# Kernel tuning notes

Hardware: AMD Instinct MI355X
Metric: run time of the kernel (lower is better)

The kernel has to match this reference:

```python
import jax, jax.numpy as jnp
import numpy as np

B, C, T, S, E = 8, 1024, 2048, 2048, 1024
SCALE = 0.7071067811865476  # sqrt(0.5), as in ConvS2S


def setup_inputs() -> dict:
    key = jax.random.key(0)
    ks = jax.random.split(key, 8)
    return {
        "conved": jax.random.normal(ks[0], (B, C, T), jnp.float32),
        "encoder_conved": jax.random.normal(ks[1], (B, S, E), jnp.float32),
        "encoder_combined": jax.random.normal(ks[2], (B, S, E), jnp.float32),
        "x": jax.random.normal(ks[3], (B, T, E), jnp.float32),
        "scale": jnp.float32(SCALE),
        # attn_hid2emb: Linear(out_channels -> emb_dim); torch weight is [out, in]
        "W_h2e": jax.random.normal(ks[4], (E, C), jnp.float32) * 0.02,
        "b_h2e": jnp.zeros((E,), jnp.float32),
        # attn_emb2hid: Linear(emb_dim -> out_channels)
        "W_e2h": jax.random.normal(ks[5], (C, E), jnp.float32) * 0.02,
        "b_e2h": jnp.zeros((C,), jnp.float32),
    }


def reference(conved, encoder_conved, encoder_combined, x, scale,
              W_h2e, b_h2e, W_e2h, b_e2h):
    # conved: [B, C, T] -> project to embedding space: [B, T, E]
    conved_emb = jnp.einsum('bct,ec->bte', conved, W_h2e) + b_h2e
    conved_combined = (conved_emb + x) * scale            # [B, T, E]
    # energy = Q @ K^T : [B, T, S]
    energy = jnp.einsum('bte,bse->bts', conved_combined, encoder_conved)
    attention = jax.nn.softmax(energy, axis=-1)           # [B, T, S]
    # attended encoding = A @ V : [B, T, E]
    attended = jnp.einsum('bts,bse->bte', attention, encoder_combined)
    # project back to hidden: [B, T, C]
    attended = jnp.einsum('bte,ce->btc', attended, W_e2h) + b_e2h
    # residual in channels-first layout: [B, C, T]
    attended_combined = conved + attended.transpose(0, 2, 1)
    return attention, attended_combined
```

## Files before the change

### kernel.cpp

```cpp
#include <hip/hip_runtime.h>
#include <hip/hip_bf16.h>

typedef unsigned short u16;
typedef __attribute__((ext_vector_type(8))) short bf16x8;
typedef __attribute__((ext_vector_type(4))) float f32x4;

#define B_ 8
#define C_ 1024
#define T_ 2048
#define S_ 2048
#define E_ 1024

__device__ __forceinline__ u16 f2bf(float v) {
    __hip_bfloat16 h = __float2bfloat16(v);
    return *reinterpret_cast<u16*>(&h);
}
__device__ __forceinline__ float bf2f(u16 u) {
    __hip_bfloat16 h = *reinterpret_cast<__hip_bfloat16*>(&u);
    return __bfloat162float(h);
}
__device__ __forceinline__ void split2(float v, u16& h, u16& l) {
    h = f2bf(v);
    l = f2bf(v - bf2f(h));
}

__device__ __forceinline__ void async16(const u16* g, u16* l) {
    __builtin_amdgcn_global_load_lds((const __attribute__((address_space(1))) void*)g,
                                     (__attribute__((address_space(3))) void*)l, 16, 0, 0);
}

template<int EPI, bool SPLIT3>
__global__ __launch_bounds__(256, 4) void gemm_bt(
    const u16* __restrict__ Ahi, const u16* __restrict__ Alo,
    const u16* __restrict__ Bhi, const u16* __restrict__ Blo,
    int Kdim, long sA, long sB, int N,
    float* __restrict__ outF, long sOutF,
    u16* __restrict__ outB, u16* __restrict__ outB2, long sOutB,
    const float* __restrict__ bias,
    const float* __restrict__ add, long sAdd,
    const float* __restrict__ scale_ptr)
{
    __shared__ u16 smem[(SPLIT3 ? 4 : 2) * 4096];
    u16* As_hi = smem;
    u16* Bs_hi = smem + 4096;
    u16* As_lo = SPLIT3 ? (smem + 8192)  : smem;
    u16* Bs_lo = SPLIT3 ? (smem + 12288) : smem;

    const int gx = gridDim.x;
    const int nwg = gx * gridDim.y;
    int f = blockIdx.y * gx + blockIdx.x;
    {
        const int q = nwg >> 3, r = nwg & 7;
        const int xcd = f & 7, idx = f >> 3;
        f = (xcd < r ? xcd * (q + 1) : r * (q + 1) + (xcd - r) * q) + idx;
    }
    const int b  = blockIdx.z;
    const int bm = (f / gx) * 128;
    const int bn = (f % gx) * 128;

    const u16* Ah = Ahi + (size_t)b * sA;
    const u16* Bh = Bhi + (size_t)b * sB;
    const u16* Al = SPLIT3 ? (Alo + (size_t)b * sA) : nullptr;
    const u16* Bl = SPLIT3 ? (Blo + (size_t)b * sB) : nullptr;

    const int tid  = threadIdx.x;
    const int w    = tid >> 6, lane = tid & 63;
    const int wr   = w >> 1,   wc   = w & 1;
    const int lr   = lane & 15, ls  = lane >> 4;

    const int srow  = lane >> 2;
    const int sslot = lane & 3;
    const int kk    = ((sslot ^ ((srow >> 1) & 3)) << 3);
    const size_t gA0 = (size_t)(bm + w * 16 + srow) * Kdim + kk;
    const size_t gA1 = (size_t)(bm + (w + 4) * 16 + srow) * Kdim + kk;
    const size_t gB0 = (size_t)(bn + w * 16 + srow) * Kdim + kk;
    const size_t gB1 = (size_t)(bn + (w + 4) * 16 + srow) * Kdim + kk;
    const int l0 = w * 512, l1 = (w + 4) * 512;

    f32x4 acc[4][4];
    #pragma unroll
    for (int m = 0; m < 4; m++) {
        #pragma unroll
        for (int n = 0; n < 4; n++) {
            f32x4 z = {0.f, 0.f, 0.f, 0.f};
            acc[m][n] = z;
        }
    }

    const int foff = ((ls ^ ((lr >> 1) & 3)) << 3);

    for (int k0 = 0; k0 < Kdim; k0 += 32) {
        async16(Ah + gA0 + k0, As_hi + l0);
        async16(Ah + gA1 + k0, As_hi + l1);
        async16(Bh + gB0 + k0, Bs_hi + l0);
        async16(Bh + gB1 + k0, Bs_hi + l1);
        if constexpr (SPLIT3) {
            async16(Al + gA0 + k0, As_lo + l0);
            async16(Al + gA1 + k0, As_lo + l1);
            async16(Bl + gB0 + k0, Bs_lo + l0);
            async16(Bl + gB1 + k0, Bs_lo + l1);
        }
        asm volatile("s_waitcnt vmcnt(0)" ::: "memory");
        __syncthreads();

        bf16x8 ah[4], al[4];
        #pragma unroll
        for (int m = 0; m < 4; m++) {
            int off = (wr * 64 + m * 16 + lr) * 32 + foff;
            ah[m] = *(const bf16x8*)(As_hi + off);
            if constexpr (SPLIT3) al[m] = *(const bf16x8*)(As_lo + off);
        }
        #pragma unroll
        for (int n = 0; n < 4; n++) {
            int off = (wc * 64 + n * 16 + lr) * 32 + foff;
            bf16x8 bh = *(const bf16x8*)(Bs_hi + off);
            if constexpr (SPLIT3) {
                bf16x8 bl = *(const bf16x8*)(Bs_lo + off);
                #pragma unroll
                for (int m = 0; m < 4; m++)
                    acc[m][n] = __builtin_amdgcn_mfma_f32_16x16x32_bf16(ah[m], bh, acc[m][n], 0, 0, 0);
                #pragma unroll
                for (int m = 0; m < 4; m++)
                    acc[m][n] = __builtin_amdgcn_mfma_f32_16x16x32_bf16(ah[m], bl, acc[m][n], 0, 0, 0);
                #pragma unroll
                for (int m = 0; m < 4; m++)
                    acc[m][n] = __builtin_amdgcn_mfma_f32_16x16x32_bf16(al[m], bh, acc[m][n], 0, 0, 0);
            } else {
                #pragma unroll
                for (int m = 0; m < 4; m++)
                    acc[m][n] = __builtin_amdgcn_mfma_f32_16x16x32_bf16(ah[m], bh, acc[m][n], 0, 0, 0);
            }
        }
        __syncthreads();
    }

    float scl = 1.0f;
    if constexpr (EPI == 0) scl = *scale_ptr;

    #pragma unroll
    for (int m = 0; m < 4; m++) {
        #pragma unroll
        for (int n = 0; n < 4; n++) {
            const int Rb = bm + wr * 64 + m * 16 + ls * 4;
            const int Cc = bn + wc * 64 + n * 16 + lr;
            f32x4 v = acc[m][n];
            #pragma unroll
            for (int j = 0; j < 4; j++) {
                const int R = Rb + j;
                const size_t o = (size_t)R * N + Cc;
                float val = v[j];
                if constexpr (EPI == 0) {
                    val = (val + bias[Cc] + add[(size_t)b * sAdd + o]) * scl;
                    u16 h, l;
                    split2(val, h, l);
                    outB[(size_t)b * sOutB + o]  = h;
                    outB2[(size_t)b * sOutB + o] = l;
                } else if constexpr (EPI == 1) {
                    outF[(size_t)b * sOutF + o] = val;
                } else if constexpr (EPI == 2) {
                    outB[(size_t)b * sOutB + o] = f2bf(val);
                } else {
                    outF[(size_t)b * sOutF + o] = val + bias[R] + add[(size_t)b * sAdd + o];
                }
            }
        }
    }
}


template<bool SPLIT>
__global__ __launch_bounds__(256) void split_cast_kernel(
    const float* __restrict__ in, u16* __restrict__ hi, u16* __restrict__ lo, long n4)
{
    long i = (long)blockIdx.x * blockDim.x + threadIdx.x;
    long stride = (long)gridDim.x * blockDim.x;
    const float4* in4 = (const float4*)in;
    ushort4* h4 = (ushort4*)hi;
    ushort4* l4 = (ushort4*)lo;
    for (; i < n4; i += stride) {
        float4 v = in4[i];
        ushort4 h, l;
        split2(v.x, h.x, l.x);
        split2(v.y, h.y, l.y);
        split2(v.z, h.z, l.z);
        split2(v.w, h.w, l.w);
        h4[i] = h;
        if constexpr (SPLIT) l4[i] = l;
    }
}

template<bool SPLIT>
__global__ __launch_bounds__(256) void transpose_split_kernel(
    const float* __restrict__ in, u16* __restrict__ hi, u16* __restrict__ lo, int R, int Cc)
{
    __shared__ float tile[32][33];
    const size_t boff = (size_t)blockIdx.z * R * Cc;
    const int c0 = blockIdx.x * 32;
    const int r0 = blockIdx.y * 32;
    const int tx = threadIdx.x;
    const int ty = threadIdx.y;

    float4 v = *(const float4*)&in[boff + (size_t)(r0 + ty) * Cc + c0 + 4 * tx];
    tile[ty][4 * tx + 0] = v.x;
    tile[ty][4 * tx + 1] = v.y;
    tile[ty][4 * tx + 2] = v.z;
    tile[ty][4 * tx + 3] = v.w;
    __syncthreads();

    ushort4 h, l;
    split2(tile[4 * tx + 0][ty], h.x, l.x);
    split2(tile[4 * tx + 1][ty], h.y, l.y);
    split2(tile[4 * tx + 2][ty], h.z, l.z);
    split2(tile[4 * tx + 3][ty], h.w, l.w);
    const size_t o = boff + (size_t)(c0 + ty) * R + r0 + 4 * tx;
    *(ushort4*)&hi[o] = h;
    if constexpr (SPLIT) *(ushort4*)&lo[o] = l;
}

__device__ __forceinline__ float wred_max(float v) {
    #pragma unroll
    for (int off = 32; off; off >>= 1) v = fmaxf(v, __shfl_xor(v, off, 64));
    return v;
}
__device__ __forceinline__ float wred_sum(float v) {
    #pragma unroll
    for (int off = 32; off; off >>= 1) v += __shfl_xor(v, off, 64);
    return v;
}

__global__ __launch_bounds__(256) void softmax_kernel(float* __restrict__ att, u16* __restrict__ attB)
{
    __shared__ float red[4];
    const size_t row = blockIdx.x;
    float* p  = att  + row * (size_t)S_;
    u16*   pb = attB + row * (size_t)S_;
    const int t = threadIdx.x, w = t >> 6, lane = t & 63;

    float4 v0 = ((const float4*)p)[t];
    float4 v1 = ((const float4*)p)[t + 256];
    float m = fmaxf(fmaxf(fmaxf(v0.x, v0.y), fmaxf(v0.z, v0.w)),
                    fmaxf(fmaxf(v1.x, v1.y), fmaxf(v1.z, v1.w)));
    m = wred_max(m);
    if (lane == 0) red[w] = m;
    __syncthreads();
    m = fmaxf(fmaxf(red[0], red[1]), fmaxf(red[2], red[3]));
    __syncthreads();

    float e0 = __expf(v0.x - m), e1 = __expf(v0.y - m), e2 = __expf(v0.z - m), e3 = __expf(v0.w - m);
    float e4 = __expf(v1.x - m), e5 = __expf(v1.y - m), e6 = __expf(v1.z - m), e7 = __expf(v1.w - m);
    float s = ((e0 + e1) + (e2 + e3)) + ((e4 + e5) + (e6 + e7));
    s = wred_sum(s);
    if (lane == 0) red[w] = s;
    __syncthreads();
    s = (red[0] + red[1]) + (red[2] + red[3]);
    const float inv = 1.0f / s;

    float4 o0 = {e0 * inv, e1 * inv, e2 * inv, e3 * inv};
    float4 o1 = {e4 * inv, e5 * inv, e6 * inv, e7 * inv};
    ((float4*)p)[t]       = o0;
    ((float4*)p)[t + 256] = o1;
    ushort4 b0, b1;
    b0.x = f2bf(o0.x); b0.y = f2bf(o0.y); b0.z = f2bf(o0.z); b0.w = f2bf(o0.w);
    b1.x = f2bf(o1.x); b1.y = f2bf(o1.y); b1.z = f2bf(o1.z); b1.w = f2bf(o1.w);
    ((ushort4*)pb)[t]       = b0;
    ((ushort4*)pb)[t + 256] = b1;
}

extern "C" void kernel_launch(void* const* d_in, const int* in_sizes, int n_in,
                              void* d_out, int out_size, void* d_ws, size_t ws_size,
                              hipStream_t stream)
{
    (void)in_sizes; (void)n_in; (void)out_size; (void)ws_size;
    const float* conved = (const float*)d_in[0];
    const float* encK   = (const float*)d_in[1];
    const float* encV   = (const float*)d_in[2];
    const float* x      = (const float*)d_in[3];
    const float* scale  = (const float*)d_in[4];
    const float* W_h2e  = (const float*)d_in[5];
    const float* b_h2e  = (const float*)d_in[6];
    const float* W_e2h  = (const float*)d_in[7];
    const float* b_e2h  = (const float*)d_in[8];

    float* attn = (float*)d_out;
    float* out2 = attn + (size_t)B_ * T_ * S_;

    const size_t NBT = (size_t)B_ * T_ * E_;
    char* p = (char*)d_ws;
    auto take = [&](size_t bytes) { char* r = p; p += bytes; return (u16*)r; };

    u16* Qhi  = take(NBT * 2);
    u16* Qlo  = take(NBT * 2);
    u16* Khi  = take(NBT * 2);
    u16* Klo  = take(NBT * 2);
    u16* Vt   = take(NBT * 2);
    u16* Whi  = take((size_t)E_ * C_ * 2);
    u16* Wlo  = take((size_t)E_ * C_ * 2);
    u16* We2h = take((size_t)C_ * E_ * 2);
    u16* CThi = take(NBT * 2);
    u16* CTlo = take(NBT * 2);
    u16* attnB = CThi;
    u16* Aemb  = Qhi;

    dim3 blk256(256);
    dim3 tblk(8, 32);

    transpose_split_kernel<true ><<<dim3(T_ / 32, C_ / 32, B_), tblk, 0, stream>>>(conved, CThi, CTlo, C_, T_);
    split_cast_kernel<true >     <<<dim3(512),  blk256, 0, stream>>>(W_h2e, Whi, Wlo, (long)E_ * C_ / 4);
    split_cast_kernel<true >     <<<dim3(2048), blk256, 0, stream>>>(encK, Khi, Klo, (long)B_ * S_ * E_ / 4);
    transpose_split_kernel<false><<<dim3(E_ / 32, S_ / 32, B_), tblk, 0, stream>>>(encV, Vt, nullptr, S_, E_);
    split_cast_kernel<false>     <<<dim3(512),  blk256, 0, stream>>>(W_e2h, We2h, nullptr, (long)C_ * E_ / 4);

    gemm_bt<0, true><<<dim3(E_ / 128, T_ / 128, B_), blk256, 0, stream>>>(
        CThi, CTlo, Whi, Wlo, C_, (long)T_ * C_, 0L, E_,
        nullptr, 0L, Qhi, Qlo, (long)T_ * E_, b_h2e, x, (long)T_ * E_, scale);

    gemm_bt<1, true><<<dim3(S_ / 128, T_ / 128, B_), blk256, 0, stream>>>(
        Qhi, Qlo, Khi, Klo, E_, (long)T_ * E_, (long)S_ * E_, S_,
        attn, (long)T_ * S_, nullptr, nullptr, 0L, nullptr, nullptr, 0L, nullptr);

    softmax_kernel<<<dim3(B_ * T_), blk256, 0, stream>>>(attn, attnB);

    gemm_bt<2, false><<<dim3(E_ / 128, T_ / 128, B_), blk256, 0, stream>>>(
        attnB, nullptr, Vt, nullptr, S_, (long)T_ * S_, (long)E_ * S_, E_,
        nullptr, 0L, Aemb, nullptr, (long)T_ * E_, nullptr, nullptr, 0L, nullptr);

    gemm_bt<3, false><<<dim3(T_ / 128, C_ / 128, B_), blk256, 0, stream>>>(
        We2h, nullptr, Aemb, nullptr, E_, 0L, (long)T_ * E_, T_,
        out2, (long)C_ * T_, nullptr, nullptr, 0L, b_e2h, conved, (long)C_ * T_, nullptr);
}
```

Measured before the change: 917.6 us.

## Drop XCD tile remap, fuse weight casts, use one wave per softmax row

```diff
diff --git a/kernel.cpp b/kernel.cpp
--- a/kernel.cpp
+++ b/kernel.cpp
@@ -46,17 +46,9 @@
     u16* As_lo = SPLIT3 ? (smem + 8192)  : smem;
     u16* Bs_lo = SPLIT3 ? (smem + 12288) : smem;
 
-    const int gx = gridDim.x;
-    const int nwg = gx * gridDim.y;
-    int f = blockIdx.y * gx + blockIdx.x;
-    {
-        const int q = nwg >> 3, r = nwg & 7;
-        const int xcd = f & 7, idx = f >> 3;
-        f = (xcd < r ? xcd * (q + 1) : r * (q + 1) + (xcd - r) * q) + idx;
-    }
     const int b  = blockIdx.z;
-    const int bm = (f / gx) * 128;
-    const int bn = (f % gx) * 128;
+    const int bm = blockIdx.y * 128;
+    const int bn = blockIdx.x * 128;
 
     const u16* Ah = Ahi + (size_t)b * sA;
     const u16* Bh = Bhi + (size_t)b * sB;
@@ -189,6 +181,32 @@
     }
 }
 
+__global__ __launch_bounds__(256) void split_weights_kernel(
+    const float* __restrict__ w1, u16* __restrict__ w1h, u16* __restrict__ w1l,
+    const float* __restrict__ w2, u16* __restrict__ w2h, long n4)
+{
+    long i = (long)blockIdx.x * blockDim.x + threadIdx.x;
+    long stride = (long)gridDim.x * blockDim.x;
+    for (; i < 2 * n4; i += stride) {
+        if (i < n4) {
+            float4 v = ((const float4*)w1)[i];
+            ushort4 h, l;
+            split2(v.x, h.x, l.x);
+            split2(v.y, h.y, l.y);
+            split2(v.z, h.z, l.z);
+            split2(v.w, h.w, l.w);
+            ((ushort4*)w1h)[i] = h;
+            ((ushort4*)w1l)[i] = l;
+        } else {
+            long j = i - n4;
+            float4 v = ((const float4*)w2)[j];
+            ushort4 h;
+            h.x = f2bf(v.x); h.y = f2bf(v.y); h.z = f2bf(v.z); h.w = f2bf(v.w);
+            ((ushort4*)w2h)[j] = h;
+        }
+    }
+}
+
 template<bool SPLIT>
 __global__ __launch_bounds__(256) void transpose_split_kernel(
     const float* __restrict__ in, u16* __restrict__ hi, u16* __restrict__ lo, int R, int Cc)
@@ -217,53 +235,50 @@
     if constexpr (SPLIT) *(ushort4*)&lo[o] = l;
 }
 
-__device__ __forceinline__ float wred_max(float v) {
-    #pragma unroll
-    for (int off = 32; off; off >>= 1) v = fmaxf(v, __shfl_xor(v, off, 64));
-    return v;
-}
-__device__ __forceinline__ float wred_sum(float v) {
-    #pragma unroll
-    for (int off = 32; off; off >>= 1) v += __shfl_xor(v, off, 64);
-    return v;
-}
-
 __global__ __launch_bounds__(256) void softmax_kernel(float* __restrict__ att, u16* __restrict__ attB)
 {
-    __shared__ float red[4];
-    const size_t row = blockIdx.x;
+    const int lane = threadIdx.x & 63;
+    const int wid  = threadIdx.x >> 6;
+    const size_t row = (size_t)blockIdx.x * 4 + wid;
     float* p  = att  + row * (size_t)S_;
     u16*   pb = attB + row * (size_t)S_;
-    const int t = threadIdx.x, w = t >> 6, lane = t & 63;
-
-    float4 v0 = ((const float4*)p)[t];
-    float4 v1 = ((const float4*)p)[t + 256];
-    float m = fmaxf(fmaxf(fmaxf(v0.x, v0.y), fmaxf(v0.z, v0.w)),
-                    fmaxf(fmaxf(v1.x, v1.y), fmaxf(v1.z, v1.w)));
-    m = wred_max(m);
-    if (lane == 0) red[w] = m;
-    __syncthreads();
-    m = fmaxf(fmaxf(red[0], red[1]), fmaxf(red[2], red[3]));
-    __syncthreads();
-
-    float e0 = __expf(v0.x - m), e1 = __expf(v0.y - m), e2 = __expf(v0.z - m), e3 = __expf(v0.w - m);
-    float e4 = __expf(v1.x - m), e5 = __expf(v1.y - m), e6 = __expf(v1.z - m), e7 = __expf(v1.w - m);
-    float s = ((e0 + e1) + (e2 + e3)) + ((e4 + e5) + (e6 + e7));
-    s = wred_sum(s);
-    if (lane == 0) red[w] = s;
-    __syncthreads();
-    s = (red[0] + red[1]) + (red[2] + red[3]);
+
+    float4 v[8];
+    #pragma unroll
+    for (int i = 0; i < 8; i++) v[i] = ((const float4*)p)[lane + 64 * i];
+
+    float m = v[0].x;
+    #pragma unroll
+    for (int i = 0; i < 8; i++)
+        m = fmaxf(m, fmaxf(fmaxf(v[i].x, v[i].y), fmaxf(v[i].z, v[i].w)));
+    #pragma unroll
+    for (int off = 32; off; off >>= 1) m = fmaxf(m, __shfl_xor(m, off, 64));
+
+    float s = 0.f;
+    #pragma unroll
+    for (int i = 0; i < 8; i++) {
+        v[i].x = __expf(v[i].x - m);
+        v[i].y = __expf(v[i].y - m);
+        v[i].z = __expf(v[i].z - m);
+        v[i].w = __expf(v[i].w - m);
+        s += (v[i].x + v[i].y) + (v[i].z + v[i].w);
+    }
+    #pragma unroll
+    for (int off = 32; off; off >>= 1) s += __shfl_xor(s, off, 64);
     const float inv = 1.0f / s;
 
-    float4 o0 = {e0 * inv, e1 * inv, e2 * inv, e3 * inv};
-    float4 o1 = {e4 * inv, e5 * inv, e6 * inv, e7 * inv};
-    ((float4*)p)[t]       = o0;
-    ((float4*)p)[t + 256] = o1;
-    ushort4 b0, b1;
-    b0.x = f2bf(o0.x); b0.y = f2bf(o0.y); b0.z = f2bf(o0.z); b0.w = f2bf(o0.w);
-    b1.x = f2bf(o1.x); b1.y = f2bf(o1.y); b1.z = f2bf(o1.z); b1.w = f2bf(o1.w);
-    ((ushort4*)pb)[t]       = b0;
-    ((ushort4*)pb)[t + 256] = b1;
+    #pragma unroll
+    for (int i = 0; i < 8; i++) {
+        float4 o;
+        o.x = v[i].x * inv;
+        o.y = v[i].y * inv;
+        o.z = v[i].z * inv;
+        o.w = v[i].w * inv;
+        ((float4*)p)[lane + 64 * i] = o;
+        ushort4 bvec;
+        bvec.x = f2bf(o.x); bvec.y = f2bf(o.y); bvec.z = f2bf(o.z); bvec.w = f2bf(o.w);
+        ((ushort4*)pb)[lane + 64 * i] = bvec;
+    }
 }
 
 extern "C" void kernel_launch(void* const* d_in, const int* in_sizes, int n_in,
@@ -305,10 +320,9 @@
     dim3 tblk(8, 32);
 
     transpose_split_kernel<true ><<<dim3(T_ / 32, C_ / 32, B_), tblk, 0, stream>>>(conved, CThi, CTlo, C_, T_);
-    split_cast_kernel<true >     <<<dim3(512),  blk256, 0, stream>>>(W_h2e, Whi, Wlo, (long)E_ * C_ / 4);
+    split_weights_kernel         <<<dim3(512),  blk256, 0, stream>>>(W_h2e, Whi, Wlo, W_e2h, We2h, (long)E_ * C_ / 4);
     split_cast_kernel<true >     <<<dim3(2048), blk256, 0, stream>>>(encK, Khi, Klo, (long)B_ * S_ * E_ / 4);
     transpose_split_kernel<false><<<dim3(E_ / 32, S_ / 32, B_), tblk, 0, stream>>>(encV, Vt, nullptr, S_, E_);
-    split_cast_kernel<false>     <<<dim3(512),  blk256, 0, stream>>>(W_e2h, We2h, nullptr, (long)C_ * E_ / 4);
 
     gemm_bt<0, true><<<dim3(E_ / 128, T_ / 128, B_), blk256, 0, stream>>>(
         CThi, CTlo, Whi, Wlo, C_, (long)T_ * C_, 0L, E_,
@@ -318,7 +332,7 @@
         Qhi, Qlo, Khi, Klo, E_, (long)T_ * E_, (long)S_ * E_, S_,
         attn, (long)T_ * S_, nullptr, nullptr, 0L, nullptr, nullptr, 0L, nullptr);
 
-    softmax_kernel<<<dim3(B_ * T_), blk256, 0, stream>>>(attn, attnB);
+    softmax_kernel<<<dim3(B_ * T_ / 4), blk256, 0, stream>>>(attn, attnB);
 
     gemm_bt<2, false><<<dim3(E_ / 128, T_ / 128, B_), blk256, 0, stream>>>(
         attnB, nullptr, Vt, nullptr, S_, (long)T_ * S_, (long)E_ * S_, E_,
```

Result: slower. 946.8 us (+3.2%).
